# Kernel optimization log

Hardware: AMD Instinct MI355X
Metric: run time of the kernel (lower is better)

## Reference

```python
import jax, jax.numpy as jnp
import numpy as np

C = 64            # multiplicity of 0e and 1o in in_irreps
N_NODES = 20000
N_EDGES = 320000
RAD_DIM = 8
HID = 64
NUM_IRREPS_OUT = 4 * C   # 2C x 0e + 2C x 1o -> 256 scalar weights
AVG_NUM_NEIGHBORS = 16.0


def setup_inputs() -> dict:
    key = jax.random.key(0)
    ks = jax.random.split(key, 10)
    node_feats = jax.random.normal(ks[0], (N_NODES, C + 3 * C), jnp.float32)
    vectors = jax.random.normal(ks[1], (N_EDGES, 3), jnp.float32)
    radial_embedding = jax.random.normal(ks[2], (N_EDGES, RAD_DIM), jnp.float32)
    senders = jax.random.randint(ks[3], (N_EDGES,), 0, N_NODES, jnp.int32)
    receivers = jax.random.randint(ks[4], (N_EDGES,), 0, N_NODES, jnp.int32)
    # e3nn-style MLP params (no bias), forward scales by 1/sqrt(fan_in)
    W0 = jax.random.normal(ks[5], (RAD_DIM, HID), jnp.float32)
    W1 = jax.random.normal(ks[6], (HID, HID), jnp.float32)
    W2 = jax.random.normal(ks[7], (HID, HID), jnp.float32)
    W3 = jax.random.normal(ks[8], (HID, NUM_IRREPS_OUT), jnp.float32)
    return {"node_feats": node_feats, "vectors": vectors,
            "radial_embedding": radial_embedding, "senders": senders,
            "receivers": receivers, "W0": W0, "W1": W1, "W2": W2, "W3": W3}


def _mlp(x, W0, W1, W2, W3):
    # MultiLayerPerceptron with gradient_normalization=1.0: scale by 1/sqrt(fan_in)
    h = jax.nn.silu(x @ W0 / jnp.sqrt(jnp.asarray(W0.shape[0], x.dtype)))
    h = jax.nn.silu(h @ W1 / jnp.sqrt(jnp.asarray(HID, x.dtype)))
    h = jax.nn.silu(h @ W2 / jnp.sqrt(jnp.asarray(HID, x.dtype)))
    return h @ W3 / jnp.sqrt(jnp.asarray(HID, x.dtype))


def reference(node_feats, vectors, radial_embedding, senders, receivers, W0, W1, W2, W3):
    n = node_feats.shape[0]
    s = node_feats[:, :C]                      # [N, C]  0e block
    v = node_feats[:, C:].reshape(n, C, 3)     # [N, C, 3]  1o block
    s_e = s[senders]                           # gather  [E, C]
    v_e = v[senders]                           # gather  [E, C, 3]
    # spherical harmonics l=1 of -vectors, normalized input, component norm
    r = -vectors
    Y = jnp.sqrt(3.0) * r / jnp.linalg.norm(r, axis=-1, keepdims=True)  # [E, 3]
    # CG tensor product filtered to target irreps (0e + 1o):
    tp_v = s_e[:, :, None] * Y[:, None, :]                 # 0e x 1o -> 1o  [E,C,3]
    tp_s = jnp.einsum('eci,ei->ec', v_e, Y) / jnp.sqrt(3.0)  # 1o x 1o -> 0e  [E,C]
    msg_s = jnp.concatenate([s_e, tp_s], axis=-1)          # [E, 2C]
    msg_v = jnp.concatenate([v_e, tp_v], axis=1)           # [E, 2C, 3]
    # per-irrep MLP gate from radial embedding
    mix = _mlp(radial_embedding, W0, W1, W2, W3)           # [E, 4C]
    msg_s = msg_s * mix[:, :2 * C]
    msg_v = msg_v * mix[:, 2 * C:, None]
    # scatter-add into receivers
    out_s = jnp.zeros((n, 2 * C), msg_s.dtype).at[receivers].add(msg_s)
    out_v = jnp.zeros((n, 2 * C, 3), msg_v.dtype).at[receivers].add(msg_v)
    out = jnp.concatenate([out_s, out_v.reshape(n, 6 * C)], axis=-1)
    return out / AVG_NUM_NEIGHBORS                         # [N, 512]
```

## Files before the change

### kernel.cpp

```cpp
#include <hip/hip_runtime.h>

typedef __attribute__((ext_vector_type(8))) short bf16x8;
typedef __attribute__((ext_vector_type(4))) float f32x4;

static __device__ __forceinline__ unsigned short f2bf(float f) {
    unsigned int u = __float_as_uint(f);
    unsigned int r = (u + 0x7fffu + ((u >> 16) & 1u)) >> 16;
    return (unsigned short)r;
}
static __device__ __forceinline__ float bf2f(unsigned short h) {
    return __uint_as_float(((unsigned int)h) << 16);
}

#define WP_TOTAL 26624

__global__ __launch_bounds__(256) void zero_kernel(int* __restrict__ p, int n)
{
    int i = blockIdx.x * 256 + threadIdx.x;
    if (i < n) p[i] = 0;
}

__global__ __launch_bounds__(256) void prep_kernel(
    const float* __restrict__ W0, const float* __restrict__ W1,
    const float* __restrict__ W2, const float* __restrict__ W3,
    unsigned short* __restrict__ Wp,
    const int* __restrict__ recv, int* __restrict__ cnt, int E)
{
    int o = blockIdx.x * 256 + threadIdx.x;
    if (o < WP_TOTAL) {
        float val;
        if (o < 2048) {
            int nt = o >> 9, w = o & 511, lane = w >> 3, j = w & 7;
            int k = (lane >> 4) * 8 + j, n = nt * 16 + (lane & 15);
            val = (k < 8) ? W0[k * 64 + n] * 0.35355339059327373f : 0.f;
        } else if (o < 6144) {
            int oo = o - 2048, fid = oo >> 9, w = oo & 511, lane = w >> 3, j = w & 7;
            int nt = fid >> 1, ks = fid & 1;
            int k = ks * 32 + (lane >> 4) * 8 + j, n = nt * 16 + (lane & 15);
            val = W1[k * 64 + n] * 0.125f;
        } else if (o < 10240) {
            int oo = o - 6144, fid = oo >> 9, w = oo & 511, lane = w >> 3, j = w & 7;
            int nt = fid >> 1, ks = fid & 1;
            int k = ks * 32 + (lane >> 4) * 8 + j, n = nt * 16 + (lane & 15);
            val = W2[k * 64 + n] * 0.125f;
        } else {
            int oo = o - 10240, fid = oo >> 9, w = oo & 511, lane = w >> 3, j = w & 7;
            int nt = fid >> 1, ks = fid & 1;
            int k = ks * 32 + (lane >> 4) * 8 + j, n = nt * 16 + (lane & 15);
            val = W3[k * 256 + n] * 0.125f;
        }
        Wp[o] = f2bf(val);
    }
    if (o < E) atomicAdd(&cnt[recv[o]], 1);
}

__global__ __launch_bounds__(1024) void scan_kernel(const int* __restrict__ cnt,
                                                    int* __restrict__ off,
                                                    int* __restrict__ cursor, int N)
{
    __shared__ int wsum[16];
    const int t = threadIdx.x, lane = t & 63, wv = t >> 6;
    const int per = (N + 1023) / 1024;
    const int base = t * per;
    int s = 0;
    for (int i = 0; i < per; ++i) { int idx = base + i; if (idx < N) s += cnt[idx]; }
    int inc = s;
    #pragma unroll
    for (int d = 1; d < 64; d <<= 1) {
        int v = __shfl_up(inc, d, 64);
        if (lane >= d) inc += v;
    }
    if (lane == 63) wsum[wv] = inc;
    __syncthreads();
    if (t == 0) {
        int run = 0;
        #pragma unroll
        for (int w = 0; w < 16; ++w) { int v = wsum[w]; wsum[w] = run; run += v; }
    }
    __syncthreads();
    int run = wsum[wv] + inc - s;
    for (int i = 0; i < per; ++i) {
        int idx = base + i;
        if (idx < N) { off[idx] = run; cursor[idx] = run; run += cnt[idx]; }
    }
    if (t == 1023) off[N] = wsum[15] + inc;
}

__global__ __launch_bounds__(256) void fill_kernel(
    const int*   __restrict__ recv,
    const int*   __restrict__ senders,
    const float* __restrict__ vectors,
    int* __restrict__ cursor,
    int* __restrict__ edge_of,
    int* __restrict__ snd_pos,
    float4* __restrict__ Y4,
    int E)
{
    int i = blockIdx.x * 256 + threadIdx.x;
    if (i < E) {
        int p = atomicAdd(&cursor[recv[i]], 1);
        edge_of[p] = i;
        snd_pos[p] = senders[i];
        float r0 = -vectors[(size_t)i * 3 + 0];
        float r1 = -vectors[(size_t)i * 3 + 1];
        float r2 = -vectors[(size_t)i * 3 + 2];
        float inv = rsqrtf(r0 * r0 + r1 * r1 + r2 * r2);
        const float s3 = 1.7320508075688772f;
        Y4[p] = make_float4(s3 * r0 * inv, s3 * r1 * inv, s3 * r2 * inv, 0.f);
    }
}

__global__ __launch_bounds__(256) void mlp_pos_kernel(
    const float* __restrict__ radial,
    const int* __restrict__ edge_of,
    const unsigned short* __restrict__ Wp,
    unsigned short* __restrict__ mix4,
    int E)
{
    __shared__ __align__(16) unsigned short sW[10240];
    __shared__ __align__(16) unsigned short sH[4][1024];

    const int t = threadIdx.x;
    {
        int4* dst = (int4*)sW;
        const int4* src = (const int4*)Wp;
        #pragma unroll
        for (int i = 0; i < 5; ++i) dst[t + i * 256] = src[t + i * 256];
    }
    __syncthreads();

    const int wv = t >> 6, l = t & 63;
    const int lrow = l & 15, quad = l >> 4;
    const int p0 = blockIdx.x * 64 + wv * 16;
    if (p0 >= E) return;

    unsigned short* H = sH[wv];

    bf16x8 afr = {0, 0, 0, 0, 0, 0, 0, 0};
    if (quad == 0) {
        int i = p0 + lrow; if (i >= E) i = E - 1;
        int e = edge_of[i];
        const float* rr = radial + (size_t)e * 8;
        float4 ra = *(const float4*)rr;
        float4 rb = *(const float4*)(rr + 4);
        afr[0] = (short)f2bf(ra.x); afr[1] = (short)f2bf(ra.y);
        afr[2] = (short)f2bf(ra.z); afr[3] = (short)f2bf(ra.w);
        afr[4] = (short)f2bf(rb.x); afr[5] = (short)f2bf(rb.y);
        afr[6] = (short)f2bf(rb.z); afr[7] = (short)f2bf(rb.w);
    }
    #pragma unroll
    for (int nt = 0; nt < 4; ++nt) {
        bf16x8 b = *(const bf16x8*)(sW + nt * 512 + l * 8);
        f32x4 z = {0.f, 0.f, 0.f, 0.f};
        f32x4 cf = __builtin_amdgcn_mfma_f32_16x16x32_bf16(afr, b, z, 0, 0, 0);
        #pragma unroll
        for (int r = 0; r < 4; ++r) {
            float v = cf[r];
            float h = v / (1.f + __expf(-v));
            int er = quad * 4 + r;
            int f  = nt * 16 + lrow;
            H[er * 64 + (f ^ ((er & 7) << 3))] = f2bf(h);
        }
    }

    #pragma unroll 1
    for (int L = 0; L < 2; ++L) {
        const unsigned short* WL = sW + 2048 + L * 4096;
        bf16x8 a[2];
        #pragma unroll
        for (int ks = 0; ks < 2; ++ks)
            a[ks] = *(const bf16x8*)(H + lrow * 64 + ((ks * 32 + quad * 8) ^ ((lrow & 7) << 3)));
        f32x4 cf[4];
        #pragma unroll
        for (int nt = 0; nt < 4; ++nt) { f32x4 z = {0.f,0.f,0.f,0.f}; cf[nt] = z; }
        #pragma unroll
        for (int ks = 0; ks < 2; ++ks) {
            #pragma unroll
            for (int nt = 0; nt < 4; ++nt) {
                bf16x8 b = *(const bf16x8*)(WL + (nt * 2 + ks) * 512 + l * 8);
                cf[nt] = __builtin_amdgcn_mfma_f32_16x16x32_bf16(a[ks], b, cf[nt], 0, 0, 0);
            }
        }
        #pragma unroll
        for (int nt = 0; nt < 4; ++nt) {
            #pragma unroll
            for (int r = 0; r < 4; ++r) {
                float v = cf[nt][r];
                float h = v / (1.f + __expf(-v));
                int er = quad * 4 + r;
                int f  = nt * 16 + lrow;
                H[er * 64 + (f ^ ((er & 7) << 3))] = f2bf(h);
            }
        }
    }

    bf16x8 a3[2];
    #pragma unroll
    for (int ks = 0; ks < 2; ++ks)
        a3[ks] = *(const bf16x8*)(H + lrow * 64 + ((ks * 32 + quad * 8) ^ ((lrow & 7) << 3)));

    const unsigned short* W3 = Wp + 10240;
    #pragma unroll 1
    for (int np = 0; np < 4; ++np) {
        f32x4 cf[4];
        #pragma unroll
        for (int g = 0; g < 4; ++g) { f32x4 z = {0.f,0.f,0.f,0.f}; cf[g] = z; }
        #pragma unroll
        for (int ks = 0; ks < 2; ++ks) {
            #pragma unroll
            for (int g = 0; g < 4; ++g) {
                int nt = g * 4 + np;
                bf16x8 b = *(const bf16x8*)(W3 + (nt * 2 + ks) * 512 + l * 8);
                cf[g] = __builtin_amdgcn_mfma_f32_16x16x32_bf16(a3[ks], b, cf[g], 0, 0, 0);
            }
        }
        int c = np * 16 + lrow;
        #pragma unroll
        for (int r = 0; r < 4; ++r) {
            int er = quad * 4 + r;
            if (p0 + er < E) {
                ushort4 u;
                u.x = f2bf(cf[0][r]); u.y = f2bf(cf[1][r]);
                u.z = f2bf(cf[2][r]); u.w = f2bf(cf[3][r]);
                *(ushort4*)&mix4[((size_t)(p0 + er) * 64 + c) * 4] = u;
            }
        }
    }
}

__global__ __launch_bounds__(256) void gather_kernel(
    const float* __restrict__ node_feats,
    const int*   __restrict__ snd_pos,
    const float4* __restrict__ Y4,
    const int*   __restrict__ off,
    const unsigned short* __restrict__ mix4,
    float* __restrict__ out, int N)
{
    int wid  = threadIdx.x >> 6;
    int lane = threadIdx.x & 63;
    int n = N - 1 - (int)(blockIdx.x * 4 + wid);
    if (n < 0) return;

    int beg = off[n], end = off[n + 1];

    float a0 = 0.f, a1 = 0.f;
    float b0 = 0.f, b1 = 0.f, b2 = 0.f;
    float c0 = 0.f, c1 = 0.f, c2 = 0.f;

    const float is3 = 0.5773502691896258f;

    #pragma unroll 4
    for (int i = beg; i < end; ++i) {
        int snd  = snd_pos[i];
        float4 Y = Y4[i];
        const float* nf = node_feats + (size_t)snd * 256;
        float s_e = nf[lane];
        float v0  = nf[64 + lane * 3 + 0];
        float v1  = nf[64 + lane * 3 + 1];
        float v2  = nf[64 + lane * 3 + 2];
        ushort4 mv = *(const ushort4*)&mix4[((size_t)i * 64 + lane) * 4];

        float m0 = bf2f(mv.x), m1 = bf2f(mv.y), m2 = bf2f(mv.z), m3 = bf2f(mv.w);

        float tp_s = (v0 * Y.x + v1 * Y.y + v2 * Y.z) * is3;

        a0 += s_e * m0;
        a1 += tp_s * m1;
        b0 += v0 * m2; b1 += v1 * m2; b2 += v2 * m2;
        float sm = s_e * m3;
        c0 += Y.x * sm; c1 += Y.y * sm; c2 += Y.z * sm;
    }

    float* o = out + (size_t)n * 512;
    const float kk = 0.0625f;
    o[lane]      = a0 * kk;
    o[64 + lane] = a1 * kk;
    o[128 + lane * 3 + 0] = b0 * kk;
    o[128 + lane * 3 + 1] = b1 * kk;
    o[128 + lane * 3 + 2] = b2 * kk;
    o[320 + lane * 3 + 0] = c0 * kk;
    o[320 + lane * 3 + 1] = c1 * kk;
    o[320 + lane * 3 + 2] = c2 * kk;
}

#define HID 64
__global__ __launch_bounds__(256) void mlp_kernel(
    const float* __restrict__ radial,
    const float* __restrict__ W0g, const float* __restrict__ W1g,
    const float* __restrict__ W2g, const float* __restrict__ W3g,
    unsigned short* __restrict__ mix, int e1)
{
    __shared__ float  sHf[HID * 256];
    __shared__ float4 sW4[1024];

    const int t = threadIdx.x;
    const int e = blockIdx.x * 256 + t;
    const bool valid = e < e1;

    if (t < 128) sW4[t] = ((const float4*)W0g)[t];
    __syncthreads();

    float x[8];
    if (valid) {
        float4 ra = ((const float4*)radial)[(size_t)e * 2 + 0];
        float4 rb = ((const float4*)radial)[(size_t)e * 2 + 1];
        x[0]=ra.x; x[1]=ra.y; x[2]=ra.z; x[3]=ra.w;
        x[4]=rb.x; x[5]=rb.y; x[6]=rb.z; x[7]=rb.w;
    } else {
        #pragma unroll
        for (int k = 0; k < 8; ++k) x[k] = 0.f;
    }

    float acc[64];
    #pragma unroll
    for (int j = 0; j < 64; ++j) acc[j] = 0.f;
    #pragma unroll
    for (int k = 0; k < 8; ++k) {
        #pragma unroll
        for (int jq = 0; jq < 16; ++jq) {
            float4 w = sW4[k * 16 + jq];
            acc[jq*4+0] = fmaf(x[k], w.x, acc[jq*4+0]);
            acc[jq*4+1] = fmaf(x[k], w.y, acc[jq*4+1]);
            acc[jq*4+2] = fmaf(x[k], w.z, acc[jq*4+2]);
            acc[jq*4+3] = fmaf(x[k], w.w, acc[jq*4+3]);
        }
    }
    #pragma unroll
    for (int j = 0; j < 64; ++j) {
        float v = acc[j] * 0.35355339059327373f;
        sHf[j * 256 + t] = v / (1.f + __expf(-v));
    }
    __syncthreads();
    #pragma unroll
    for (int i = 0; i < 4; ++i) sW4[t + i * 256] = ((const float4*)W1g)[t + i * 256];
    __syncthreads();

    #pragma unroll
    for (int j = 0; j < 64; ++j) acc[j] = 0.f;
    #pragma unroll 2
    for (int k = 0; k < 64; ++k) {
        float hk = sHf[k * 256 + t];
        #pragma unroll
        for (int jq = 0; jq < 16; ++jq) {
            float4 w = sW4[k * 16 + jq];
            acc[jq*4+0] = fmaf(hk, w.x, acc[jq*4+0]);
            acc[jq*4+1] = fmaf(hk, w.y, acc[jq*4+1]);
            acc[jq*4+2] = fmaf(hk, w.z, acc[jq*4+2]);
            acc[jq*4+3] = fmaf(hk, w.w, acc[jq*4+3]);
        }
    }
    __syncthreads();
    #pragma unroll
    for (int i = 0; i < 4; ++i) sW4[t + i * 256] = ((const float4*)W2g)[t + i * 256];
    #pragma unroll
    for (int j = 0; j < 64; ++j) {
        float v = acc[j] * 0.125f;
        sHf[j * 256 + t] = v / (1.f + __expf(-v));
    }
    __syncthreads();

    #pragma unroll
    for (int j = 0; j < 64; ++j) acc[j] = 0.f;
    #pragma unroll 2
    for (int k = 0; k < 64; ++k) {
        float hk = sHf[k * 256 + t];
        #pragma unroll
        for (int jq = 0; jq < 16; ++jq) {
            float4 w = sW4[k * 16 + jq];
            acc[jq*4+0] = fmaf(hk, w.x, acc[jq*4+0]);
            acc[jq*4+1] = fmaf(hk, w.y, acc[jq*4+1]);
            acc[jq*4+2] = fmaf(hk, w.z, acc[jq*4+2]);
            acc[jq*4+3] = fmaf(hk, w.w, acc[jq*4+3]);
        }
    }
    __syncthreads();
    #pragma unroll
    for (int j = 0; j < 64; ++j) {
        float v = acc[j] * 0.125f;
        sHf[j * 256 + t] = v / (1.f + __expf(-v));
    }

    unsigned short* mrow = mix + (size_t)e * 256;
    #pragma unroll 1
    for (int jt = 0; jt < 4; ++jt) {
        #pragma unroll
        for (int i = 0; i < 4; ++i) {
            int m = t + i * 256;
            sW4[m] = ((const float4*)W3g)[(m >> 4) * 64 + jt * 16 + (m & 15)];
        }
        __syncthreads();

        #pragma unroll
        for (int j = 0; j < 64; ++j) acc[j] = 0.f;
        #pragma unroll 2
        for (int k = 0; k < 64; ++k) {
            float hk = sHf[k * 256 + t];
            #pragma unroll
            for (int jq = 0; jq < 16; ++jq) {
                float4 w = sW4[k * 16 + jq];
                acc[jq*4+0] = fmaf(hk, w.x, acc[jq*4+0]);
                acc[jq*4+1] = fmaf(hk, w.y, acc[jq*4+1]);
                acc[jq*4+2] = fmaf(hk, w.z, acc[jq*4+2]);
                acc[jq*4+3] = fmaf(hk, w.w, acc[jq*4+3]);
            }
        }
        if (valid) {
            #pragma unroll
            for (int j4 = 0; j4 < 16; ++j4) {
                ushort4 u;
                u.x = f2bf(acc[j4*4+0] * 0.125f);
                u.y = f2bf(acc[j4*4+1] * 0.125f);
                u.z = f2bf(acc[j4*4+2] * 0.125f);
                u.w = f2bf(acc[j4*4+3] * 0.125f);
                *reinterpret_cast<ushort4*>(&mrow[jt * 64 + j4 * 4]) = u;
            }
        }
        __syncthreads();
    }
}

__global__ __launch_bounds__(256) void scatter_kernel(
    const float* __restrict__ node_feats,
    const float* __restrict__ vectors,
    const int*   __restrict__ senders,
    const int*   __restrict__ receivers,
    const unsigned short* __restrict__ mix,
    float* __restrict__ out, int e0, int e1)
{
    int wid  = threadIdx.x >> 6;
    int lane = threadIdx.x & 63;
    int e = e0 + blockIdx.x * 4 + wid;
    if (e >= e1) return;

    int snd = senders[e];
    int rcv = receivers[e];

    float r0 = -vectors[(size_t)e * 3 + 0];
    float r1 = -vectors[(size_t)e * 3 + 1];
    float r2 = -vectors[(size_t)e * 3 + 2];
    float inv = rsqrtf(r0 * r0 + r1 * r1 + r2 * r2);
    float Y0 = 1.7320508075688772f * r0 * inv;
    float Y1 = 1.7320508075688772f * r1 * inv;
    float Y2 = 1.7320508075688772f * r2 * inv;

    const float* nf = node_feats + (size_t)snd * 256;
    float s_e = nf[lane];
    float v0 = nf[64 + lane * 3 + 0];
    float v1 = nf[64 + lane * 3 + 1];
    float v2 = nf[64 + lane * 3 + 2];

    float tp_s = (v0 * Y0 + v1 * Y1 + v2 * Y2) * 0.5773502691896258f;

    const unsigned short* m = mix + (size_t)(e - e0) * 256;
    float m0 = bf2f(m[lane]), m1 = bf2f(m[64 + lane]);
    float m2 = bf2f(m[128 + lane]), m3 = bf2f(m[192 + lane]);

    float* orow = out + (size_t)rcv * 512;
    const float kk = 0.0625f;
    atomicAdd(&orow[lane],      s_e  * m0 * kk);
    atomicAdd(&orow[64 + lane], tp_s * m1 * kk);
    float mv = m2 * kk;
    atomicAdd(&orow[128 + lane * 3 + 0], v0 * mv);
    atomicAdd(&orow[128 + lane * 3 + 1], v1 * mv);
    atomicAdd(&orow[128 + lane * 3 + 2], v2 * mv);
    float ms = s_e * m3 * kk;
    atomicAdd(&orow[320 + lane * 3 + 0], Y0 * ms);
    atomicAdd(&orow[320 + lane * 3 + 1], Y1 * ms);
    atomicAdd(&orow[320 + lane * 3 + 2], Y2 * ms);
}

extern "C" void kernel_launch(void* const* d_in, const int* in_sizes, int n_in,
                              void* d_out, int out_size, void* d_ws, size_t ws_size,
                              hipStream_t stream)
{
    const float* node_feats = (const float*)d_in[0];
    const float* vectors    = (const float*)d_in[1];
    const float* radial     = (const float*)d_in[2];
    const int*   senders    = (const int*)d_in[3];
    const int*   receivers  = (const int*)d_in[4];
    const float* W0         = (const float*)d_in[5];
    const float* W1         = (const float*)d_in[6];
    const float* W2         = (const float*)d_in[7];
    const float* W3         = (const float*)d_in[8];
    float* out = (float*)d_out;

    const int E = in_sizes[3];
    const int N = in_sizes[0] / 256;

    size_t mix_bytes = (size_t)E * 64 * 4 * sizeof(unsigned short);
    size_t mix_al    = (mix_bytes + 255) & ~(size_t)255;
    size_t int_bytes = (size_t)(N + (N + 1) + N + E + E) * sizeof(int);
    size_t int_al    = (int_bytes + 255) & ~(size_t)255;
    size_t y4_bytes  = (size_t)E * sizeof(float4);
    size_t y4_al     = (y4_bytes + 255) & ~(size_t)255;
    size_t wp_bytes  = (size_t)WP_TOTAL * sizeof(unsigned short);
    size_t need      = mix_al + int_al + y4_al + wp_bytes;

    if (ws_size >= need) {
        unsigned short* mix4 = (unsigned short*)d_ws;
        int* cnt      = (int*)((char*)d_ws + mix_al);
        int* off      = cnt + N;
        int* cursor   = off + (N + 1);
        int* edge_of  = cursor + N;
        int* snd_pos  = edge_of + E;
        float4* Y4    = (float4*)((char*)d_ws + mix_al + int_al);
        unsigned short* Wp = (unsigned short*)((char*)d_ws + mix_al + int_al + y4_al);

        zero_kernel<<<dim3((N + 255) / 256), dim3(256), 0, stream>>>(cnt, N);

        prep_kernel<<<dim3((E + 255) / 256), dim3(256), 0, stream>>>(
            W0, W1, W2, W3, Wp, receivers, cnt, E);
        scan_kernel<<<dim3(1), dim3(1024), 0, stream>>>(cnt, off, cursor, N);
        fill_kernel<<<dim3((E + 255) / 256), dim3(256), 0, stream>>>(
            receivers, senders, vectors, cursor, edge_of, snd_pos, Y4, E);

        mlp_pos_kernel<<<dim3((E + 63) / 64), dim3(256), 0, stream>>>(
            radial, edge_of, Wp, mix4, E);

        gather_kernel<<<dim3((N + 3) / 4), dim3(256), 0, stream>>>(
            node_feats, snd_pos, Y4, off, mix4, out, N);
    } else {
        hipMemsetAsync(d_out, 0, (size_t)out_size * sizeof(float), stream);
        size_t per_edge = 256 * sizeof(unsigned short);
        long long chunk_ll = (long long)(ws_size / per_edge);
        int chunk = (chunk_ll > E) ? E : (int)chunk_ll;
        chunk &= ~255;
        if (chunk <= 0) chunk = 256;
        unsigned short* mix = (unsigned short*)d_ws;
        for (int s = 0; s < E; s += chunk) {
            int eend = s + chunk; if (eend > E) eend = E;
            int ne = eend - s;
            mlp_kernel<<<dim3((ne + 255) / 256), dim3(256), 0, stream>>>(
                radial + (size_t)s * 8, W0, W1, W2, W3, mix, ne);
            scatter_kernel<<<dim3((ne + 3) / 4), dim3(256), 0, stream>>>(
                node_feats, vectors, senders, receivers, mix, out, s, eend);
        }
    }
}
```

Baseline: 217.4 us.

## Process four receiver nodes per wavefront in gather kernel for more memory parallelism

Each wavefront now handles four consecutive receiver nodes at once, stepping through their edge lists together and issuing four independent sets of gathers per iteration. Past the end of its own list a node's loads are clamped to its last edge and its contribution is masked to zero. The intent is to raise memory-level parallelism and hide gather latency. In exchange, degree imbalance adds wasted loads, register pressure rises (with launch_bounds set to 4), the grid is four times smaller, and the reversed node order is dropped.

```diff
diff --git a/kernel.cpp b/kernel.cpp
--- a/kernel.cpp
+++ b/kernel.cpp
@@ -228,7 +228,7 @@
     }
 }
 
-__global__ __launch_bounds__(256) void gather_kernel(
+__global__ __launch_bounds__(256, 4) void gather_kernel(
     const float* __restrict__ node_feats,
     const int*   __restrict__ snd_pos,
     const float4* __restrict__ Y4,
@@ -236,51 +236,109 @@
     const unsigned short* __restrict__ mix4,
     float* __restrict__ out, int N)
 {
-    int wid  = threadIdx.x >> 6;
-    int lane = threadIdx.x & 63;
-    int n = N - 1 - (int)(blockIdx.x * 4 + wid);
-    if (n < 0) return;
-
-    int beg = off[n], end = off[n + 1];
-
-    float a0 = 0.f, a1 = 0.f;
-    float b0 = 0.f, b1 = 0.f, b2 = 0.f;
-    float c0 = 0.f, c1 = 0.f, c2 = 0.f;
+    const int wid  = threadIdx.x >> 6;
+    const int lane = threadIdx.x & 63;
+    const int nb = (blockIdx.x * 4 + wid) * 4;
+    if (nb >= N) return;
+
+    const int n0 = nb;
+    const int n1 = (nb + 1 < N) ? nb + 1 : N - 1;
+    const int n2 = (nb + 2 < N) ? nb + 2 : N - 1;
+    const int n3 = (nb + 3 < N) ? nb + 3 : N - 1;
+
+    const int beg0 = off[n0], d0 = off[n0 + 1] - beg0;
+    const int beg1 = off[n1], d1 = off[n1 + 1] - beg1;
+    const int beg2 = off[n2], d2 = off[n2 + 1] - beg2;
+    const int beg3 = off[n3], d3 = off[n3 + 1] - beg3;
+
+    int maxd = d0;
+    maxd = (d1 > maxd) ? d1 : maxd;
+    maxd = (d2 > maxd) ? d2 : maxd;
+    maxd = (d3 > maxd) ? d3 : maxd;
+
+    float A0[8] = {0,0,0,0,0,0,0,0};
+    float A1[8] = {0,0,0,0,0,0,0,0};
+    float A2[8] = {0,0,0,0,0,0,0,0};
+    float A3[8] = {0,0,0,0,0,0,0,0};
 
     const float is3 = 0.5773502691896258f;
 
-    #pragma unroll 4
-    for (int i = beg; i < end; ++i) {
-        int snd  = snd_pos[i];
-        float4 Y = Y4[i];
-        const float* nf = node_feats + (size_t)snd * 256;
-        float s_e = nf[lane];
-        float v0  = nf[64 + lane * 3 + 0];
-        float v1  = nf[64 + lane * 3 + 1];
-        float v2  = nf[64 + lane * 3 + 2];
-        ushort4 mv = *(const ushort4*)&mix4[((size_t)i * 64 + lane) * 4];
-
-        float m0 = bf2f(mv.x), m1 = bf2f(mv.y), m2 = bf2f(mv.z), m3 = bf2f(mv.w);
-
-        float tp_s = (v0 * Y.x + v1 * Y.y + v2 * Y.z) * is3;
-
-        a0 += s_e * m0;
-        a1 += tp_s * m1;
-        b0 += v0 * m2; b1 += v1 * m2; b2 += v2 * m2;
-        float sm = s_e * m3;
-        c0 += Y.x * sm; c1 += Y.y * sm; c2 += Y.z * sm;
-    }
-
-    float* o = out + (size_t)n * 512;
+    for (int k = 0; k < maxd; ++k) {
+        int p0 = (d0 > 0) ? beg0 + ((k < d0) ? k : d0 - 1) : 0;
+        int p1 = (d1 > 0) ? beg1 + ((k < d1) ? k : d1 - 1) : 0;
+        int p2 = (d2 > 0) ? beg2 + ((k < d2) ? k : d2 - 1) : 0;
+        int p3 = (d3 > 0) ? beg3 + ((k < d3) ? k : d3 - 1) : 0;
+        float w0 = (k < d0) ? 1.f : 0.f;
+        float w1 = (k < d1) ? 1.f : 0.f;
+        float w2 = (k < d2) ? 1.f : 0.f;
+        float w3 = (k < d3) ? 1.f : 0.f;
+
+        int s0 = snd_pos[p0], s1 = snd_pos[p1], s2 = snd_pos[p2], s3 = snd_pos[p3];
+        float4 Ya = Y4[p0], Yb = Y4[p1], Yc = Y4[p2], Yd = Y4[p3];
+        ushort4 ma = *(const ushort4*)&mix4[((size_t)p0 * 64 + lane) * 4];
+        ushort4 mb = *(const ushort4*)&mix4[((size_t)p1 * 64 + lane) * 4];
+        ushort4 mc = *(const ushort4*)&mix4[((size_t)p2 * 64 + lane) * 4];
+        ushort4 md = *(const ushort4*)&mix4[((size_t)p3 * 64 + lane) * 4];
+        const float* f0p = node_feats + (size_t)s0 * 256;
+        const float* f1p = node_feats + (size_t)s1 * 256;
+        const float* f2p = node_feats + (size_t)s2 * 256;
+        const float* f3p = node_feats + (size_t)s3 * 256;
+        float se0 = f0p[lane], se1 = f1p[lane], se2 = f2p[lane], se3 = f3p[lane];
+        float v00 = f0p[64+lane*3], v01 = f0p[65+lane*3], v02 = f0p[66+lane*3];
+        float v10 = f1p[64+lane*3], v11 = f1p[65+lane*3], v12 = f1p[66+lane*3];
+        float v20 = f2p[64+lane*3], v21 = f2p[65+lane*3], v22 = f2p[66+lane*3];
+        float v30 = f3p[64+lane*3], v31 = f3p[65+lane*3], v32 = f3p[66+lane*3];
+
+        {
+            float m0 = bf2f(ma.x)*w0, m1 = bf2f(ma.y)*w0, m2 = bf2f(ma.z)*w0, m3 = bf2f(ma.w)*w0;
+            float tp = (v00*Ya.x + v01*Ya.y + v02*Ya.z) * is3;
+            A0[0] += se0*m0;  A0[1] += tp*m1;
+            A0[2] += v00*m2;  A0[3] += v01*m2;  A0[4] += v02*m2;
+            float sm = se0*m3;
+            A0[5] += Ya.x*sm; A0[6] += Ya.y*sm; A0[7] += Ya.z*sm;
+        }
+        {
+            float m0 = bf2f(mb.x)*w1, m1 = bf2f(mb.y)*w1, m2 = bf2f(mb.z)*w1, m3 = bf2f(mb.w)*w1;
+            float tp = (v10*Yb.x + v11*Yb.y + v12*Yb.z) * is3;
+            A1[0] += se1*m0;  A1[1] += tp*m1;
+            A1[2] += v10*m2;  A1[3] += v11*m2;  A1[4] += v12*m2;
+            float sm = se1*m3;
+            A1[5] += Yb.x*sm; A1[6] += Yb.y*sm; A1[7] += Yb.z*sm;
+        }
+        {
+            float m0 = bf2f(mc.x)*w2, m1 = bf2f(mc.y)*w2, m2 = bf2f(mc.z)*w2, m3 = bf2f(mc.w)*w2;
+            float tp = (v20*Yc.x + v21*Yc.y + v22*Yc.z) * is3;
+            A2[0] += se2*m0;  A2[1] += tp*m1;
+            A2[2] += v20*m2;  A2[3] += v21*m2;  A2[4] += v22*m2;
+            float sm = se2*m3;
+            A2[5] += Yc.x*sm; A2[6] += Yc.y*sm; A2[7] += Yc.z*sm;
+        }
+        {
+            float m0 = bf2f(md.x)*w3, m1 = bf2f(md.y)*w3, m2 = bf2f(md.z)*w3, m3 = bf2f(md.w)*w3;
+            float tp = (v30*Yd.x + v31*Yd.y + v32*Yd.z) * is3;
+            A3[0] += se3*m0;  A3[1] += tp*m1;
+            A3[2] += v30*m2;  A3[3] += v31*m2;  A3[4] += v32*m2;
+            float sm = se3*m3;
+            A3[5] += Yd.x*sm; A3[6] += Yd.y*sm; A3[7] += Yd.z*sm;
+        }
+    }
+
     const float kk = 0.0625f;
-    o[lane]      = a0 * kk;
-    o[64 + lane] = a1 * kk;
-    o[128 + lane * 3 + 0] = b0 * kk;
-    o[128 + lane * 3 + 1] = b1 * kk;
-    o[128 + lane * 3 + 2] = b2 * kk;
-    o[320 + lane * 3 + 0] = c0 * kk;
-    o[320 + lane * 3 + 1] = c1 * kk;
-    o[320 + lane * 3 + 2] = c2 * kk;
+    #pragma unroll
+    for (int j = 0; j < 4; ++j) {
+        int n = nb + j;
+        if (n >= N) break;
+        const float* A = (j == 0) ? A0 : (j == 1) ? A1 : (j == 2) ? A2 : A3;
+        float* o = out + (size_t)n * 512;
+        o[lane]      = A[0] * kk;
+        o[64 + lane] = A[1] * kk;
+        o[128 + lane * 3 + 0] = A[2] * kk;
+        o[128 + lane * 3 + 1] = A[3] * kk;
+        o[128 + lane * 3 + 2] = A[4] * kk;
+        o[320 + lane * 3 + 0] = A[5] * kk;
+        o[320 + lane * 3 + 1] = A[6] * kk;
+        o[320 + lane * 3 + 2] = A[7] * kk;
+    }
 }
 
 #define HID 64
@@ -517,7 +575,7 @@
         mlp_pos_kernel<<<dim3((E + 63) / 64), dim3(256), 0, stream>>>(
             radial, edge_of, Wp, mix4, E);
 
-        gather_kernel<<<dim3((N + 3) / 4), dim3(256), 0, stream>>>(
+        gather_kernel<<<dim3((N + 15) / 16), dim3(256), 0, stream>>>(
             node_feats, snd_pos, Y4, off, mix4, out, N);
     } else {
         hipMemsetAsync(d_out, 0, (size_t)out_size * sizeof(float), stream);
```

Measured after the change: 238.5 us. 1.1x slower.
